# Optimization experiments

Measured on AMD Instinct MI355X. Metric: run time of the kernel, lower is better.

## Reference

```python
import jax, jax.numpy as jnp
import numpy as np

B, CIN, COUT, H, W = 8, 64, 64, 96, 96
K = 3
PAD = 1
BN_EPS = 1e-5


def conv2d(x, w, b):
    # plain 3x3 conv, stride 1, pad 1 (NCHW / OIHW)
    y = jax.lax.conv_general_dilated(
        x, w, window_strides=(1, 1), padding=[(PAD, PAD), (PAD, PAD)],
        dimension_numbers=("NCHW", "OIHW", "NCHW"))
    return y + b[None, :, None, None]


def setup_inputs() -> dict:
    key = jax.random.key(0)
    ks = jax.random.split(key, 6)
    s = 0.05  # small init so offsets stay near the regular grid (matches DCN zero-ish init)
    return {
        "x": jax.random.normal(ks[0], (B, CIN, H, W), jnp.float32),
        "offset_w": jax.random.normal(ks[1], (2 * K * K, CIN, K, K), jnp.float32) * s,
        "offset_b": jnp.zeros((2 * K * K,), jnp.float32),
        "mod_w": jax.random.normal(ks[2], (K * K, CIN, K, K), jnp.float32) * s,
        "mod_b": jnp.zeros((K * K,), jnp.float32),
        "weight": jax.random.normal(ks[3], (COUT, CIN, K, K), jnp.float32) * s,
        "bias": jax.random.normal(ks[4], (COUT,), jnp.float32) * s,
        "bn_gamma": jnp.ones((COUT,), jnp.float32),
        "bn_beta": jnp.zeros((COUT,), jnp.float32),
        "bn_mean": jnp.zeros((COUT,), jnp.float32),
        "bn_var": jnp.ones((COUT,), jnp.float32),
    }


def _deform_sample(xb, py, px):
    # xb: [C,H,W]; py, px: [K2,H,W] fractional sampling coords (zero outside image)
    y0 = jnp.floor(py)
    x0 = jnp.floor(px)
    dy = py - y0
    dx = px - x0

    def gather(yi, xi):
        valid = ((yi >= 0) & (yi < H) & (xi >= 0) & (xi < W)).astype(xb.dtype)
        yc = jnp.clip(yi, 0, H - 1).astype(jnp.int32)
        xc = jnp.clip(xi, 0, W - 1).astype(jnp.int32)
        return xb[:, yc, xc] * valid  # [C,K2,H,W]

    v00 = gather(y0, x0)
    v01 = gather(y0, x0 + 1.0)
    v10 = gather(y0 + 1.0, x0)
    v11 = gather(y0 + 1.0, x0 + 1.0)
    return (v00 * (1 - dy) * (1 - dx) + v01 * (1 - dy) * dx
            + v10 * dy * (1 - dx) + v11 * dy * dx)  # [C,K2,H,W]


def reference(x, offset_w, offset_b, mod_w, mod_b, weight, bias,
              bn_gamma, bn_beta, bn_mean, bn_var):
    # 1) predict offsets and modulation mask (DCNv2)
    offset = conv2d(x, offset_w, offset_b)                 # [B, 2*K2, H, W]
    modulator = 2.0 * jax.nn.sigmoid(conv2d(x, mod_w, mod_b))  # [B, K2, H, W]

    off = offset.reshape(B, K * K, 2, H, W)
    off_y, off_x = off[:, :, 0], off[:, :, 1]              # [B,K2,H,W]

    # 2) base sampling grid per kernel tap
    ky, kx = jnp.meshgrid(jnp.arange(K), jnp.arange(K), indexing="ij")
    base_y = (jnp.arange(H)[None, :, None] - PAD
              + ky.reshape(-1)[:, None, None]).astype(jnp.float32)  # [K2,H,1]
    base_x = (jnp.arange(W)[None, None, :] - PAD
              + kx.reshape(-1)[:, None, None]).astype(jnp.float32)  # [K2,1,W]
    py = base_y + off_y                                    # [B,K2,H,W]
    px = base_x + off_x

    # 3) bilinear gather at irregular positions, modulate per tap
    sampled = jax.vmap(_deform_sample)(x, py, px)          # [B,C,K2,H,W]
    sampled = sampled * modulator[:, None]                 # broadcast over C

    # 4) contract taps with the regular conv weight
    wk = weight.reshape(COUT, CIN, K * K)
    y = jnp.einsum("bckhw,ock->bohw", sampled, wk) + bias[None, :, None, None]

    # 5) BatchNorm (inference: running stats) + ReLU
    inv = bn_gamma / jnp.sqrt(bn_var + BN_EPS)
    y = (y - bn_mean[None, :, None, None]) * inv[None, :, None, None] \
        + bn_beta[None, :, None, None]
    return jax.nn.relu(y)
```

## Files before the change

kernel.cpp:

```cpp
#include <hip/hip_runtime.h>
#include <hip/hip_bf16.h>
#include <hip/hip_fp16.h>
#include <math.h>

#define BB 8
#define HH 96
#define WW 96
#define HW 9216
#define BN_EPS 1e-5f

typedef _Float16 f16x2 __attribute__((ext_vector_type(2)));
typedef _Float16 f16x8 __attribute__((ext_vector_type(8)));
typedef float f32x4 __attribute__((ext_vector_type(4)));

union HU  { _Float16 h; unsigned short u; };
union UH2 { unsigned u; f16x2 h; };
union U4H { uint4 u; f16x2 h2[4]; };

#define OFF_W4   0
#define SZ_W4    (BB*9*HW*16)
#define OFF_XT   (OFF_W4 + SZ_W4)
#define SZ_XT    (BB*HW*64*2)
#define OFF_XY   (OFF_XT + SZ_XT)
#define SZ_XY    (BB*9*HW*4)
#define OFF_WB   (OFF_XY + SZ_XY)
#define SZ_WB    (64*576*2)
#define OFF_WO   (OFF_WB + SZ_WB)
#define SZ_WO    (32*576*2)
#define OFF_BN   (OFF_WO + SZ_WO)
#define SZ_BN    (64*2*4)

__global__ __launch_bounds__(256) void prep_kernel(
    const float* __restrict__ weight, const float* __restrict__ offw,
    const float* __restrict__ modw,
    const float* __restrict__ bias, const float* __restrict__ gamma,
    const float* __restrict__ beta, const float* __restrict__ mean,
    const float* __restrict__ var,
    _Float16* __restrict__ wB, _Float16* __restrict__ wOff,
    float* __restrict__ bnS, float* __restrict__ bnB) {
  int tid = blockIdx.x * 256 + threadIdx.x;
  if (tid < 64 * 576) {
    int o = tid / 576, ck = tid % 576;
    int k = ck >> 6, c = ck & 63;
    wB[tid] = (_Float16)weight[o * 576 + c * 9 + k];
  }
  int t2 = tid - 64 * 576;
  if (t2 >= 0 && t2 < 32 * 576) {
    int oc = t2 / 576, kcol = t2 % 576;
    int kk = kcol >> 6, c = kcol & 63;
    float v = 0.f;
    if (oc < 18)      v = offw[(oc * 64 + c) * 9 + kk];
    else if (oc < 27) v = modw[((oc - 18) * 64 + c) * 9 + kk];
    wOff[t2] = (_Float16)v;
  }
  int t3 = tid - (64 * 576 + 32 * 576);
  if (t3 >= 0 && t3 < 64) {
    float inv = gamma[t3] * rsqrtf(var[t3] + BN_EPS);
    bnS[t3] = inv;
    bnB[t3] = (bias[t3] - mean[t3]) * inv + beta[t3];
  }
}

__global__ __launch_bounds__(256) void transpose_x_kernel(
    const float* __restrict__ x, _Float16* __restrict__ xT) {
  __shared__ float tile[64][65];
  int tid = threadIdx.x;
  int b = blockIdx.x & 7;
  int hwb = (blockIdx.x >> 3) * 64;
  int col = tid & 63, g = tid >> 6;
  float r[16];
#pragma unroll
  for (int it = 0; it < 16; ++it)
    r[it] = x[(b * 64 + it * 4 + g) * HW + hwb + col];
  __builtin_amdgcn_sched_barrier(0);
#pragma unroll
  for (int it = 0; it < 16; ++it)
    tile[it * 4 + g][col] = r[it];
  __syncthreads();
#pragma unroll
  for (int it = 0; it < 16; ++it) {
    int p = it * 4 + g;
    xT[(size_t)(b * HW + hwb + p) * 64 + col] = (_Float16)tile[col][p];
  }
}

__device__ __forceinline__ unsigned rep16(float w) {
  HU cv; cv.h = (_Float16)w;
  return 0x10001u * (unsigned)cv.u;
}

__global__ __launch_bounds__(256, 8) void conv_offsets_kernel(
    const _Float16* __restrict__ xTh, const _Float16* __restrict__ wOff,
    const float* __restrict__ offb, const float* __restrict__ modb,
    uint4* __restrict__ w4, unsigned* __restrict__ xy) {
  __shared__ __attribute__((aligned(16))) _Float16 sN[3 * 34 * 70];
  __shared__ float o_off[32 * 33];

  int tid = threadIdx.x;
  int lane = tid & 63;
  int wv = __builtin_amdgcn_readfirstlane(tid >> 6);

  int bi = blockIdx.x;
  int b = bi & 7, rem = bi >> 3;
  int h = rem / 3, w0 = (rem % 3) * 32;

  const _Float16* xb = xTh + (size_t)b * HW * 64;
  _Float16 sv[26];
#pragma unroll
  for (int i = 0; i < 26; ++i) {
    int p = wv + 4 * i;
    _Float16 v = (_Float16)0.f;
    if (p < 102) {
      int row = p / 34, col = p - row * 34;
      int y = h + row - 1, xx = w0 + col - 1;
      if ((y >= 0) && (y < HH) && (xx >= 0) && (xx < WW))
        v = xb[(size_t)(y * WW + xx) * 64 + lane];
    }
    sv[i] = v;
  }
  __builtin_amdgcn_sched_barrier(0);
#pragma unroll
  for (int i = 0; i < 26; ++i) {
    int p = wv + 4 * i;
    if (p < 102) {
      int row = p / 34, col = p - row * 34;
      sN[(row * 34 + col) * 70 + lane] = sv[i];
    }
  }
  __syncthreads();

  int r = lane & 15, g = lane >> 4;
  int mt = wv >> 1, nt = wv & 1;
  int px = mt * 16 + r;
  const _Float16* bp = wOff + (nt * 16 + r) * 576 + g * 8;
  f32x4 acc = {0.f, 0.f, 0.f, 0.f};
#pragma unroll
  for (int s = 0; s < 18; ++s) {
    int kk = s >> 1, ky = kk / 3, kx = kk - ky * 3;
    f16x8 a = *(const f16x8*)&sN[(ky * 34 + px + kx) * 70 + (s & 1) * 32 + g * 8];
    f16x8 bb = *(const f16x8*)(bp + s * 32);
    acc = __builtin_amdgcn_mfma_f32_16x16x32_f16(a, bb, acc, 0, 0, 0);
  }
#pragma unroll
  for (int j = 0; j < 4; ++j)
    o_off[(mt * 16 + g * 4 + j) * 33 + nt * 16 + r] = acc[j];
  __syncthreads();

  for (int it = tid; it < 288; it += 256) {
    int pxx = it & 31, k = it >> 5;
    int ky = k / 3, kx = k - ky * 3;
    int w = w0 + pxx;

    float offy = o_off[pxx * 33 + 2 * k]     + offb[2 * k];
    float offx = o_off[pxx * 33 + 2 * k + 1] + offb[2 * k + 1];
    float mod  = 2.f / (1.f + __expf(-(o_off[pxx * 33 + 18 + k] + modb[k])));

    float py  = (float)(h - 1 + ky) + offy;
    float px_ = (float)(w - 1 + kx) + offx;
    float y0f = floorf(py), x0f = floorf(px_);
    float dy = py - y0f, dx = px_ - x0f;
    int y0 = (int)y0f, x0 = (int)x0f;
    int y1 = y0 + 1, x1 = x0 + 1;
    bool vy0 = (y0 >= 0) && (y0 < HH), vy1 = (y1 >= 0) && (y1 < HH);
    bool vx0 = (x0 >= 0) && (x0 < WW), vx1 = (x1 >= 0) && (x1 < WW);
    float w00 = (vy0 && vx0) ? (1.f - dy) * (1.f - dx) * mod : 0.f;
    float w01 = (vy0 && vx1) ? (1.f - dy) * dx * mod : 0.f;
    float w10 = (vy1 && vx0) ? dy * (1.f - dx) * mod : 0.f;
    float w11 = (vy1 && vx1) ? dy * dx * mod : 0.f;
    int y0c = min(max(y0, 0), HH - 1), y1c = min(max(y1, 0), HH - 1);
    int x0c = min(max(x0, 0), WW - 1), x1c = min(max(x1, 0), WW - 1);
    unsigned pk = (unsigned)y0c | ((unsigned)y1c << 8) |
                  ((unsigned)x0c << 16) | ((unsigned)x1c << 24);
    int idx = (b * 9 + k) * HW + h * WW + w;
    w4[idx] = make_uint4(rep16(w00), rep16(w01), rep16(w10), rep16(w11));
    xy[idx] = pk;
  }
}

__global__ __launch_bounds__(256, 6) void dcn_main_kernel(
    const _Float16* __restrict__ xT,
    const uint4* __restrict__ w4pk, const unsigned* __restrict__ xy,
    const _Float16* __restrict__ wB,
    const float* __restrict__ bnS, const float* __restrict__ bnB,
    float* __restrict__ out) {
  __shared__ __attribute__((aligned(16))) _Float16 s_A[16 * 584];
  __shared__ uint4 w4s[4][36];
  float* o_lds = (float*)s_A;

  int tid = threadIdx.x;
  int lane = tid & 63;
  int wv = __builtin_amdgcn_readfirstlane(tid >> 6);

  int bi = blockIdx.x;
  int b = bi & 7, t = bi >> 3;
  int h = t / 6, w0 = (t - (t / 6) * 6) * 16;
  int hwrow = h * WW + w0;

  const unsigned char* xbc = (const unsigned char*)(xT + (size_t)b * HW * 64);

  if (lane < 36) {
    int px = lane / 9, k = lane - px * 9;
    w4s[wv][lane] = w4pk[(b * 9 + k) * HW + hwrow + wv * 4 + px];
  }

  int hsel = lane >> 5;
  unsigned ch4 = (unsigned)((lane & 31) << 2);

#pragma unroll
  for (int px = 0; px < 4; ++px) {
    int pl = wv * 4 + px;
    int hw = hwrow + pl;
    unsigned q[9];
#pragma unroll
    for (int k = 0; k < 9; ++k) q[k] = xy[(b * 9 + k) * HW + hw];

#pragma unroll
    for (int p4 = 0; p4 < 4; ++p4) {
      const int kA = 2 * p4;
      unsigned qa = q[kA], qb = q[kA + 1];
      unsigned aY0 = qa & 255u, aY1 = (qa >> 8) & 255u;
      unsigned aX0 = (qa >> 16) & 255u, aX1 = qa >> 24;
      unsigned bY0 = qb & 255u, bY1 = (qb >> 8) & 255u;
      unsigned bX0 = (qb >> 16) & 255u, bX1 = qb >> 24;
      unsigned oA0 = (aY0 * WW + aX0) << 7, oA1 = (aY0 * WW + aX1) << 7;
      unsigned oA2 = (aY1 * WW + aX0) << 7, oA3 = (aY1 * WW + aX1) << 7;
      unsigned oB0 = (bY0 * WW + bX0) << 7, oB1 = (bY0 * WW + bX1) << 7;
      unsigned oB2 = (bY1 * WW + bX0) << 7, oB3 = (bY1 * WW + bX1) << 7;
      unsigned a0 = (hsel ? oB0 : oA0) + ch4;
      unsigned a1 = (hsel ? oB1 : oA1) + ch4;
      unsigned a2 = (hsel ? oB2 : oA2) + ch4;
      unsigned a3 = (hsel ? oB3 : oA3) + ch4;
      unsigned t0 = *(const unsigned*)(xbc + a0);
      unsigned t1 = *(const unsigned*)(xbc + a1);
      unsigned t2 = *(const unsigned*)(xbc + a2);
      unsigned t3 = *(const unsigned*)(xbc + a3);
      U4H W; W.u = w4s[wv][px * 9 + kA + hsel];
      UH2 v0, v1, v2, v3, s;
      v0.u = t0; v1.u = t1; v2.u = t2; v3.u = t3;
      s.h = v0.h * W.h2[0] + v1.h * W.h2[1] + v2.h * W.h2[2] + v3.h * W.h2[3];
      *(unsigned*)&s_A[pl * 584 + (kA + hsel) * 64 + (int)(ch4 >> 1)] = s.u;
    }
    {
      unsigned qa = q[8];
      unsigned aY0 = qa & 255u, aY1 = (qa >> 8) & 255u;
      unsigned aX0 = (qa >> 16) & 255u, aX1 = qa >> 24;
      unsigned a0 = (((aY0 * WW + aX0) << 7)) + ch4;
      unsigned a1 = (((aY0 * WW + aX1) << 7)) + ch4;
      unsigned a2 = (((aY1 * WW + aX0) << 7)) + ch4;
      unsigned a3 = (((aY1 * WW + aX1) << 7)) + ch4;
      unsigned t0 = *(const unsigned*)(xbc + a0);
      unsigned t1 = *(const unsigned*)(xbc + a1);
      unsigned t2 = *(const unsigned*)(xbc + a2);
      unsigned t3 = *(const unsigned*)(xbc + a3);
      U4H W; W.u = w4s[wv][px * 9 + 8];
      UH2 v0, v1, v2, v3, s;
      v0.u = t0; v1.u = t1; v2.u = t2; v3.u = t3;
      s.h = v0.h * W.h2[0] + v1.h * W.h2[1] + v2.h * W.h2[2] + v3.h * W.h2[3];
      if (lane < 32)
        *(unsigned*)&s_A[pl * 584 + 512 + (int)(ch4 >> 1)] = s.u;
    }
  }
  __syncthreads();

  int r = lane & 15, g = lane >> 4;
  const _Float16* arow = s_A + r * 584 + g * 8;
  const _Float16* bp = wB + (wv * 16 + r) * 576 + g * 8;
  f32x4 accA = {0.f, 0.f, 0.f, 0.f}, accB = {0.f, 0.f, 0.f, 0.f};
#pragma unroll 3
  for (int s = 0; s < 18; s += 2) {
    f16x8 a0 = *(const f16x8*)(arow + s * 32);
    f16x8 b0 = *(const f16x8*)(bp + s * 32);
    f16x8 a1 = *(const f16x8*)(arow + s * 32 + 32);
    f16x8 b1 = *(const f16x8*)(bp + s * 32 + 32);
    accA = __builtin_amdgcn_mfma_f32_16x16x32_f16(a0, b0, accA, 0, 0, 0);
    accB = __builtin_amdgcn_mfma_f32_16x16x32_f16(a1, b1, accB, 0, 0, 0);
  }

  int o = wv * 16 + r;
  float sc = bnS[o], sh = bnB[o];
  __syncthreads();
#pragma unroll
  for (int j = 0; j < 4; ++j) {
    int px = g * 4 + j;
    o_lds[o * 20 + px] = fmaxf((accA[j] + accB[j]) * sc + sh, 0.f);
  }
  __syncthreads();

  int oo = tid >> 2, q = tid & 3;
  float4 u = *(const float4*)&o_lds[oo * 20 + q * 4];
  *(float4*)(out + (size_t)(b * 64 + oo) * HW + hwrow + q * 4) = u;
}

extern "C" void kernel_launch(void* const* d_in, const int* in_sizes, int n_in,
                              void* d_out, int out_size, void* d_ws, size_t ws_size,
                              hipStream_t stream) {
  const float* x      = (const float*)d_in[0];
  const float* offw   = (const float*)d_in[1];
  const float* offb   = (const float*)d_in[2];
  const float* modw   = (const float*)d_in[3];
  const float* modb   = (const float*)d_in[4];
  const float* weight = (const float*)d_in[5];
  const float* bias   = (const float*)d_in[6];
  const float* gamma  = (const float*)d_in[7];
  const float* beta   = (const float*)d_in[8];
  const float* mean   = (const float*)d_in[9];
  const float* var    = (const float*)d_in[10];

  char* ws = (char*)d_ws;
  uint4*     w4    = (uint4*)(ws + OFF_W4);
  _Float16*  xTh   = (_Float16*)(ws + OFF_XT);
  unsigned*  xybuf = (unsigned*)(ws + OFF_XY);
  _Float16*  wB    = (_Float16*)(ws + OFF_WB);
  _Float16*  wOff  = (_Float16*)(ws + OFF_WO);
  float*     bnS   = (float*)(ws + OFF_BN);
  float*     bnB   = bnS + 64;

  prep_kernel<<<217, 256, 0, stream>>>(weight, offw, modw, bias, gamma, beta,
                                       mean, var, wB, wOff, bnS, bnB);
  transpose_x_kernel<<<1152, 256, 0, stream>>>(x, xTh);
  conv_offsets_kernel<<<2304, 256, 0, stream>>>(xTh, wOff, offb, modb, w4, xybuf);
  dcn_main_kernel<<<4608, 256, 0, stream>>>(xTh, w4, xybuf, wB, bnS, bnB,
                                            (float*)d_out);
}
```

Baseline: 102.1 us.

## Store precomputed gather offsets in tile-ordered records and reduce bilinear taps via shuffles

```diff
diff --git a/kernel.cpp b/kernel.cpp
--- a/kernel.cpp
+++ b/kernel.cpp
@@ -15,15 +15,14 @@
 
 union HU  { _Float16 h; unsigned short u; };
 union UH2 { unsigned u; f16x2 h; };
-union U4H { uint4 u; f16x2 h2[4]; };
-
-#define OFF_W4   0
-#define SZ_W4    (BB*9*HW*16)
-#define OFF_XT   (OFF_W4 + SZ_W4)
+
+#define OFF_MO   0
+#define SZ_MO    (BB*576*144*16)
+#define OFF_MW   (OFF_MO + SZ_MO)
+#define SZ_MW    (BB*576*144*16)
+#define OFF_XT   (OFF_MW + SZ_MW)
 #define SZ_XT    (BB*HW*64*2)
-#define OFF_XY   (OFF_XT + SZ_XT)
-#define SZ_XY    (BB*9*HW*4)
-#define OFF_WB   (OFF_XY + SZ_XY)
+#define OFF_WB   (OFF_XT + SZ_XT)
 #define SZ_WB    (64*576*2)
 #define OFF_WO   (OFF_WB + SZ_WB)
 #define SZ_WO    (32*576*2)
@@ -92,7 +91,7 @@
 __global__ __launch_bounds__(256, 8) void conv_offsets_kernel(
     const _Float16* __restrict__ xTh, const _Float16* __restrict__ wOff,
     const float* __restrict__ offb, const float* __restrict__ modb,
-    uint4* __restrict__ w4, unsigned* __restrict__ xy) {
+    uint4* __restrict__ metaOFF, uint4* __restrict__ metaW4) {
   __shared__ __attribute__((aligned(16))) _Float16 sN[3 * 34 * 70];
   __shared__ float o_off[32 * 33];
 
@@ -169,22 +168,26 @@
     float w11 = (vy1 && vx1) ? dy * dx * mod : 0.f;
     int y0c = min(max(y0, 0), HH - 1), y1c = min(max(y1, 0), HH - 1);
     int x0c = min(max(x0, 0), WW - 1), x1c = min(max(x1, 0), WW - 1);
-    unsigned pk = (unsigned)y0c | ((unsigned)y1c << 8) |
-                  ((unsigned)x0c << 16) | ((unsigned)x1c << 24);
-    int idx = (b * 9 + k) * HW + h * WW + w;
-    w4[idx] = make_uint4(rep16(w00), rep16(w01), rep16(w10), rep16(w11));
-    xy[idx] = pk;
+
+    int tdcn = h * 6 + (w0 >> 4) + (pxx >> 4);
+    int rec = ((b * 576 + tdcn) * 16 + (pxx & 15)) * 9 + k;
+    metaOFF[rec] = make_uint4((unsigned)((y0c * WW + x0c) << 7),
+                              (unsigned)((y0c * WW + x1c) << 7),
+                              (unsigned)((y1c * WW + x0c) << 7),
+                              (unsigned)((y1c * WW + x1c) << 7));
+    metaW4[rec]  = make_uint4(rep16(w00), rep16(w01), rep16(w10), rep16(w11));
   }
 }
 
 __global__ __launch_bounds__(256, 6) void dcn_main_kernel(
     const _Float16* __restrict__ xT,
-    const uint4* __restrict__ w4pk, const unsigned* __restrict__ xy,
+    const uint4* __restrict__ metaOFF, const uint4* __restrict__ metaW4,
     const _Float16* __restrict__ wB,
     const float* __restrict__ bnS, const float* __restrict__ bnB,
     float* __restrict__ out) {
   __shared__ __attribute__((aligned(16))) _Float16 s_A[16 * 584];
-  __shared__ uint4 w4s[4][36];
+  __shared__ __attribute__((aligned(16))) uint4 m_off[144];
+  __shared__ __attribute__((aligned(16))) uint4 m_w4[144];
   float* o_lds = (float*)s_A;
 
   int tid = threadIdx.x;
@@ -198,66 +201,40 @@
 
   const unsigned char* xbc = (const unsigned char*)(xT + (size_t)b * HW * 64);
 
-  if (lane < 36) {
-    int px = lane / 9, k = lane - px * 9;
-    w4s[wv][lane] = w4pk[(b * 9 + k) * HW + hwrow + wv * 4 + px];
-  }
-
-  int hsel = lane >> 5;
-  unsigned ch4 = (unsigned)((lane & 31) << 2);
+  int base = (b * 576 + t) * 144;
+  if (tid < 144) m_off[tid] = metaOFF[base + tid];
+  int t2 = tid - 144;
+  if (t2 >= 0) m_w4[t2] = metaW4[base + t2];
+  if (tid < 32) m_w4[112 + tid] = metaW4[base + 112 + tid];
+  __syncthreads();
+
+  const unsigned* offw32 = (const unsigned*)m_off;
+  const unsigned* w4w32  = (const unsigned*)m_w4;
+  int tsel = (lane >> 3) & 3;
+  unsigned chB = (unsigned)(((lane >> 5) << 6) | ((lane & 7) << 3));
+  int c0 = ((lane >> 5) << 5) | ((lane & 7) << 2);
+  bool wlane = (lane & 24) == 0;
 
 #pragma unroll
   for (int px = 0; px < 4; ++px) {
     int pl = wv * 4 + px;
-    int hw = hwrow + pl;
-    unsigned q[9];
-#pragma unroll
-    for (int k = 0; k < 9; ++k) q[k] = xy[(b * 9 + k) * HW + hw];
-
-#pragma unroll
-    for (int p4 = 0; p4 < 4; ++p4) {
-      const int kA = 2 * p4;
-      unsigned qa = q[kA], qb = q[kA + 1];
-      unsigned aY0 = qa & 255u, aY1 = (qa >> 8) & 255u;
-      unsigned aX0 = (qa >> 16) & 255u, aX1 = qa >> 24;
-      unsigned bY0 = qb & 255u, bY1 = (qb >> 8) & 255u;
-      unsigned bX0 = (qb >> 16) & 255u, bX1 = qb >> 24;
-      unsigned oA0 = (aY0 * WW + aX0) << 7, oA1 = (aY0 * WW + aX1) << 7;
-      unsigned oA2 = (aY1 * WW + aX0) << 7, oA3 = (aY1 * WW + aX1) << 7;
-      unsigned oB0 = (bY0 * WW + bX0) << 7, oB1 = (bY0 * WW + bX1) << 7;
-      unsigned oB2 = (bY1 * WW + bX0) << 7, oB3 = (bY1 * WW + bX1) << 7;
-      unsigned a0 = (hsel ? oB0 : oA0) + ch4;
-      unsigned a1 = (hsel ? oB1 : oA1) + ch4;
-      unsigned a2 = (hsel ? oB2 : oA2) + ch4;
-      unsigned a3 = (hsel ? oB3 : oA3) + ch4;
-      unsigned t0 = *(const unsigned*)(xbc + a0);
-      unsigned t1 = *(const unsigned*)(xbc + a1);
-      unsigned t2 = *(const unsigned*)(xbc + a2);
-      unsigned t3 = *(const unsigned*)(xbc + a3);
-      U4H W; W.u = w4s[wv][px * 9 + kA + hsel];
-      UH2 v0, v1, v2, v3, s;
-      v0.u = t0; v1.u = t1; v2.u = t2; v3.u = t3;
-      s.h = v0.h * W.h2[0] + v1.h * W.h2[1] + v2.h * W.h2[2] + v3.h * W.h2[3];
-      *(unsigned*)&s_A[pl * 584 + (kA + hsel) * 64 + (int)(ch4 >> 1)] = s.u;
-    }
-    {
-      unsigned qa = q[8];
-      unsigned aY0 = qa & 255u, aY1 = (qa >> 8) & 255u;
-      unsigned aX0 = (qa >> 16) & 255u, aX1 = qa >> 24;
-      unsigned a0 = (((aY0 * WW + aX0) << 7)) + ch4;
-      unsigned a1 = (((aY0 * WW + aX1) << 7)) + ch4;
-      unsigned a2 = (((aY1 * WW + aX0) << 7)) + ch4;
-      unsigned a3 = (((aY1 * WW + aX1) << 7)) + ch4;
-      unsigned t0 = *(const unsigned*)(xbc + a0);
-      unsigned t1 = *(const unsigned*)(xbc + a1);
-      unsigned t2 = *(const unsigned*)(xbc + a2);
-      unsigned t3 = *(const unsigned*)(xbc + a3);
-      U4H W; W.u = w4s[wv][px * 9 + 8];
-      UH2 v0, v1, v2, v3, s;
-      v0.u = t0; v1.u = t1; v2.u = t2; v3.u = t3;
-      s.h = v0.h * W.h2[0] + v1.h * W.h2[1] + v2.h * W.h2[2] + v3.h * W.h2[3];
-      if (lane < 32)
-        *(unsigned*)&s_A[pl * 584 + 512 + (int)(ch4 >> 1)] = s.u;
+#pragma unroll
+    for (int k = 0; k < 9; ++k) {
+      int rec = (pl * 9 + k) * 4 + tsel;
+      unsigned toff = offw32[rec];
+      unsigned wsel = w4w32[rec];
+      uint2 v = *(const uint2*)(xbc + toff + chB);
+      UH2 a0, a1, wz, r0, r1, s0, s1;
+      a0.u = v.x; a1.u = v.y; wz.u = wsel;
+      r0.h = a0.h * wz.h; r1.h = a1.h * wz.h;
+      s0.u = __shfl_xor((int)r0.u, 8);
+      s1.u = __shfl_xor((int)r1.u, 8);
+      r0.h += s0.h; r1.h += s1.h;
+      s0.u = __shfl_xor((int)r0.u, 16);
+      s1.u = __shfl_xor((int)r1.u, 16);
+      r0.h += s0.h; r1.h += s1.h;
+      if (wlane)
+        *(uint2*)&s_A[pl * 584 + k * 64 + c0] = make_uint2(r0.u, r1.u);
     }
   }
   __syncthreads();
@@ -307,18 +284,19 @@
   const float* var    = (const float*)d_in[10];
 
   char* ws = (char*)d_ws;
-  uint4*     w4    = (uint4*)(ws + OFF_W4);
-  _Float16*  xTh   = (_Float16*)(ws + OFF_XT);
-  unsigned*  xybuf = (unsigned*)(ws + OFF_XY);
-  _Float16*  wB    = (_Float16*)(ws + OFF_WB);
-  _Float16*  wOff  = (_Float16*)(ws + OFF_WO);
-  float*     bnS   = (float*)(ws + OFF_BN);
-  float*     bnB   = bnS + 64;
+  uint4*     metaOFF = (uint4*)(ws + OFF_MO);
+  uint4*     metaW4  = (uint4*)(ws + OFF_MW);
+  _Float16*  xTh     = (_Float16*)(ws + OFF_XT);
+  _Float16*  wB      = (_Float16*)(ws + OFF_WB);
+  _Float16*  wOff    = (_Float16*)(ws + OFF_WO);
+  float*     bnS     = (float*)(ws + OFF_BN);
+  float*     bnB     = bnS + 64;
 
   prep_kernel<<<217, 256, 0, stream>>>(weight, offw, modw, bias, gamma, beta,
                                        mean, var, wB, wOff, bnS, bnB);
   transpose_x_kernel<<<1152, 256, 0, stream>>>(x, xTh);
-  conv_offsets_kernel<<<2304, 256, 0, stream>>>(xTh, wOff, offb, modb, w4, xybuf);
-  dcn_main_kernel<<<4608, 256, 0, stream>>>(xTh, w4, xybuf, wB, bnS, bnB,
+  conv_offsets_kernel<<<2304, 256, 0, stream>>>(xTh, wOff, offb, modb,
+                                                metaOFF, metaW4);
+  dcn_main_kernel<<<4608, 256, 0, stream>>>(xTh, metaOFF, metaW4, wB, bnS, bnB,
                                             (float*)d_out);
 }
```

Result: slower. 123.8 us (+21.2%).
